# Kernel tuning notes

Measured on AMD Instinct MI355X. Metric: run time of the kernel, lower is better.

## Reference

```python
import jax, jax.numpy as jnp
import numpy as np

N_NODES = 1_000_000
HIDDEN = 256
NUM_GRAPHS = 1024
EPS = 1e-6


def setup_inputs() -> dict:
    key = jax.random.key(0)
    k1, k2 = jax.random.split(key)
    x = jax.random.normal(k1, (N_NODES, HIDDEN), dtype=jnp.float32)
    batch = jnp.sort(jax.random.randint(k2, (N_NODES,), 0, NUM_GRAPHS, dtype=jnp.int64))
    weight = jnp.ones((HIDDEN,), dtype=jnp.float32)
    return {"x": x, "batch": batch, "weight": weight}


def reference(x, batch, weight):
    # scatter_mean(x**2, batch, dim=0): per-graph mean of squared features
    seg_sum = jax.ops.segment_sum(x * x, batch, num_segments=NUM_GRAPHS)  # [G, H]
    counts = jax.ops.segment_sum(jnp.ones((x.shape[0],), x.dtype), batch,
                                 num_segments=NUM_GRAPHS)  # [G]
    seg_mean = seg_sum / jnp.maximum(counts, 1.0)[:, None]  # [G, H]
    rms_squared = seg_mean[batch]  # gather back to nodes: [N, H]
    rms = jnp.sqrt(jnp.mean(rms_squared, axis=-1, keepdims=True) + EPS)  # [N, 1]
    return weight * (x / rms)
```

## Files before the change

### kernel.cpp

```cpp
#include <hip/hip_runtime.h>

#define HIDDEN 256
#define NGRAPH 1024
#define EPS 1e-6f
#define STAGE_ROWS 152

typedef float f32x4 __attribute__((ext_vector_type(4)));

__global__ __launch_bounds__(512) void k_fused(
    const float* __restrict__ x, const int* __restrict__ batch,
    const float* __restrict__ w, float* __restrict__ out, int n_nodes) {

    __shared__ float smem[STAGE_ROWS * HIDDEN + 8];

    const int g    = (int)blockIdx.x;
    const int tid  = (int)threadIdx.x;
    const int lane = tid & 63;
    const int wid  = tid >> 6;

    int lo = 0, hi = n_nodes;
    while (lo < hi) { int m = (lo + hi) >> 1; if (batch[m] < g) lo = m + 1; else hi = m; }
    const int start = lo;
    int lo2 = start, hi2 = n_nodes;
    while (lo2 < hi2) { int m = (lo2 + hi2) >> 1; if (batch[m] < g + 1) lo2 = m + 1; else hi2 = m; }
    const int count = lo2 - start;
    if (count <= 0) return;

    const int nsweep = (count + 63) >> 6;

    float acc = 0.0f;
    for (int s = 0; s < nsweep; ++s) {
        const int base = (s << 6) + (wid << 3);
        if (base + 8 <= count) {
            f32x4 v[8];
            #pragma unroll
            for (int k = 0; k < 8; ++k)
                v[k] = *reinterpret_cast<const f32x4*>(
                    x + (size_t)(start + base + k) * HIDDEN + (size_t)lane * 4);
            if (base + 8 <= STAGE_ROWS) {
                #pragma unroll
                for (int k = 0; k < 8; ++k)
                    *reinterpret_cast<f32x4*>(
                        &smem[(base + k) * HIDDEN + lane * 4]) = v[k];
            }
            #pragma unroll
            for (int k = 0; k < 8; ++k)
                acc += v[k].x * v[k].x + v[k].y * v[k].y + v[k].z * v[k].z + v[k].w * v[k].w;
        } else {
            for (int r = base; r < count; ++r) {
                const f32x4 v = *reinterpret_cast<const f32x4*>(
                    x + (size_t)(start + r) * HIDDEN + (size_t)lane * 4);
                acc += v.x * v.x + v.y * v.y + v.z * v.z + v.w * v.w;
            }
        }
    }
    #pragma unroll
    for (int off = 32; off > 0; off >>= 1)
        acc += __shfl_xor(acc, off);
    if (lane == 0) smem[STAGE_ROWS * HIDDEN + wid] = acc;
    __syncthreads();

    float total = 0.0f;
    #pragma unroll
    for (int k = 0; k < 8; ++k) total += smem[STAGE_ROWS * HIDDEN + k];
    const float mean = total / ((float)count * (float)HIDDEN);
    const float rr   = 1.0f / sqrtf(mean + EPS);

    const f32x4 wv = *reinterpret_cast<const f32x4*>(w + (size_t)lane * 4);
    for (int s = nsweep - 1; s >= 0; --s) {
        const int base = (s << 6) + (wid << 3);
        if (base + 8 <= count) {
            f32x4 v[8];
            if (base + 8 <= STAGE_ROWS) {
                #pragma unroll
                for (int k = 0; k < 8; ++k)
                    v[k] = *reinterpret_cast<const f32x4*>(
                        &smem[(base + k) * HIDDEN + lane * 4]);
            } else {
                #pragma unroll
                for (int k = 0; k < 8; ++k)
                    v[k] = __builtin_nontemporal_load(reinterpret_cast<const f32x4*>(
                        x + (size_t)(start + base + k) * HIDDEN + (size_t)lane * 4));
            }
            #pragma unroll
            for (int k = 0; k < 8; ++k) {
                f32x4 o;
                o.x = v[k].x * wv.x * rr;
                o.y = v[k].y * wv.y * rr;
                o.z = v[k].z * wv.z * rr;
                o.w = v[k].w * wv.w * rr;
                __builtin_nontemporal_store(o, reinterpret_cast<f32x4*>(
                    out + (size_t)(start + base + k) * HIDDEN + (size_t)lane * 4));
            }
        } else {
            for (int r = base; r < count; ++r) {
                const f32x4 v = __builtin_nontemporal_load(reinterpret_cast<const f32x4*>(
                    x + (size_t)(start + r) * HIDDEN + (size_t)lane * 4));
                f32x4 o;
                o.x = v.x * wv.x * rr;
                o.y = v.y * wv.y * rr;
                o.z = v.z * wv.z * rr;
                o.w = v.w * wv.w * rr;
                __builtin_nontemporal_store(o, reinterpret_cast<f32x4*>(
                    out + (size_t)(start + r) * HIDDEN + (size_t)lane * 4));
            }
        }
    }
}

extern "C" void kernel_launch(void* const* d_in, const int* in_sizes, int n_in,
                              void* d_out, int out_size, void* d_ws, size_t ws_size,
                              hipStream_t stream) {
    const float* x     = (const float*)d_in[0];
    const int*   batch = (const int*)d_in[1];
    const float* w     = (const float*)d_in[2];
    float*       out   = (float*)d_out;
    const int n_nodes  = in_sizes[1];

    k_fused<<<NGRAPH, 512, 0, stream>>>(x, batch, w, out, n_nodes);
}
```

Before: 443.4 us.

## Stage segment rows in registers plus smaller LDS buffer to avoid re-reads

The kernel now caches the first two 64-row sweeps of each graph segment in LDS and the next five sweeps in per-thread registers (40 f32x4 per thread), rather than 152 rows in LDS. The normalize pass writes those staged rows straight from registers or LDS and only re-reads the rows beyond them from global memory. Launch bounds now request 2 blocks per CU. Segments average about 977 rows, so most rows are still read twice. The goal is to stage more of each segment (448 rows versus 152) and cut HBM re-reads, at the cost of high register pressure that may cause spills or limit occupancy.

```diff
diff --git a/kernel.cpp b/kernel.cpp
--- a/kernel.cpp
+++ b/kernel.cpp
@@ -3,15 +3,21 @@
 #define HIDDEN 256
 #define NGRAPH 1024
 #define EPS 1e-6f
-#define STAGE_ROWS 152
+#define LDS_SWEEPS 2
+#define REG_SWEEPS 5
+#define STAGE_SWEEPS (LDS_SWEEPS + REG_SWEEPS)
 
 typedef float f32x4 __attribute__((ext_vector_type(4)));
 
-__global__ __launch_bounds__(512) void k_fused(
+__device__ __forceinline__ float ssum(const f32x4 v) {
+    return v.x * v.x + v.y * v.y + v.z * v.z + v.w * v.w;
+}
+
+__global__ __launch_bounds__(512, 2) void k_fused(
     const float* __restrict__ x, const int* __restrict__ batch,
     const float* __restrict__ w, float* __restrict__ out, int n_nodes) {
 
-    __shared__ float smem[STAGE_ROWS * HIDDEN + 8];
+    __shared__ float smem[LDS_SWEEPS * 64 * HIDDEN + 8];
 
     const int g    = (int)blockIdx.x;
     const int tid  = (int)threadIdx.x;
@@ -29,7 +35,45 @@
     const int nsweep = (count + 63) >> 6;
 
     float acc = 0.0f;
-    for (int s = 0; s < nsweep; ++s) {
+    f32x4 rv[REG_SWEEPS][8];
+
+    #pragma unroll
+    for (int s = 0; s < LDS_SWEEPS; ++s) {
+        const int base = (s << 6) + (wid << 3);
+        if (base + 8 <= count) {
+            f32x4 v[8];
+            #pragma unroll
+            for (int k = 0; k < 8; ++k)
+                v[k] = __builtin_nontemporal_load(reinterpret_cast<const f32x4*>(
+                    x + (size_t)(start + base + k) * HIDDEN + (size_t)lane * 4));
+            #pragma unroll
+            for (int k = 0; k < 8; ++k)
+                *reinterpret_cast<f32x4*>(&smem[(base + k) * HIDDEN + lane * 4]) = v[k];
+            #pragma unroll
+            for (int k = 0; k < 8; ++k) acc += ssum(v[k]);
+        } else {
+            for (int r = base; r < count; ++r)
+                acc += ssum(*reinterpret_cast<const f32x4*>(
+                    x + (size_t)(start + r) * HIDDEN + (size_t)lane * 4));
+        }
+    }
+    #pragma unroll
+    for (int j = 0; j < REG_SWEEPS; ++j) {
+        const int base = ((LDS_SWEEPS + j) << 6) + (wid << 3);
+        if (base + 8 <= count) {
+            #pragma unroll
+            for (int k = 0; k < 8; ++k)
+                rv[j][k] = __builtin_nontemporal_load(reinterpret_cast<const f32x4*>(
+                    x + (size_t)(start + base + k) * HIDDEN + (size_t)lane * 4));
+            #pragma unroll
+            for (int k = 0; k < 8; ++k) acc += ssum(rv[j][k]);
+        } else {
+            for (int r = base; r < count; ++r)
+                acc += ssum(*reinterpret_cast<const f32x4*>(
+                    x + (size_t)(start + r) * HIDDEN + (size_t)lane * 4));
+        }
+    }
+    for (int s = STAGE_SWEEPS; s < nsweep; ++s) {
         const int base = (s << 6) + (wid << 3);
         if (base + 8 <= count) {
             f32x4 v[8];
@@ -37,58 +81,41 @@
             for (int k = 0; k < 8; ++k)
                 v[k] = *reinterpret_cast<const f32x4*>(
                     x + (size_t)(start + base + k) * HIDDEN + (size_t)lane * 4);
-            if (base + 8 <= STAGE_ROWS) {
-                #pragma unroll
-                for (int k = 0; k < 8; ++k)
-                    *reinterpret_cast<f32x4*>(
-                        &smem[(base + k) * HIDDEN + lane * 4]) = v[k];
-            }
             #pragma unroll
-            for (int k = 0; k < 8; ++k)
-                acc += v[k].x * v[k].x + v[k].y * v[k].y + v[k].z * v[k].z + v[k].w * v[k].w;
+            for (int k = 0; k < 8; ++k) acc += ssum(v[k]);
         } else {
-            for (int r = base; r < count; ++r) {
-                const f32x4 v = *reinterpret_cast<const f32x4*>(
-                    x + (size_t)(start + r) * HIDDEN + (size_t)lane * 4);
-                acc += v.x * v.x + v.y * v.y + v.z * v.z + v.w * v.w;
-            }
+            for (int r = base; r < count; ++r)
+                acc += ssum(*reinterpret_cast<const f32x4*>(
+                    x + (size_t)(start + r) * HIDDEN + (size_t)lane * 4));
         }
     }
+
     #pragma unroll
     for (int off = 32; off > 0; off >>= 1)
         acc += __shfl_xor(acc, off);
-    if (lane == 0) smem[STAGE_ROWS * HIDDEN + wid] = acc;
+    if (lane == 0) smem[LDS_SWEEPS * 64 * HIDDEN + wid] = acc;
     __syncthreads();
 
     float total = 0.0f;
     #pragma unroll
-    for (int k = 0; k < 8; ++k) total += smem[STAGE_ROWS * HIDDEN + k];
+    for (int k = 0; k < 8; ++k) total += smem[LDS_SWEEPS * 64 * HIDDEN + k];
     const float mean = total / ((float)count * (float)HIDDEN);
     const float rr   = 1.0f / sqrtf(mean + EPS);
 
     const f32x4 wv = *reinterpret_cast<const f32x4*>(w + (size_t)lane * 4);
-    for (int s = nsweep - 1; s >= 0; --s) {
+
+    for (int s = nsweep - 1; s >= STAGE_SWEEPS; --s) {
         const int base = (s << 6) + (wid << 3);
         if (base + 8 <= count) {
             f32x4 v[8];
-            if (base + 8 <= STAGE_ROWS) {
-                #pragma unroll
-                for (int k = 0; k < 8; ++k)
-                    v[k] = *reinterpret_cast<const f32x4*>(
-                        &smem[(base + k) * HIDDEN + lane * 4]);
-            } else {
-                #pragma unroll
-                for (int k = 0; k < 8; ++k)
-                    v[k] = __builtin_nontemporal_load(reinterpret_cast<const f32x4*>(
-                        x + (size_t)(start + base + k) * HIDDEN + (size_t)lane * 4));
-            }
+            #pragma unroll
+            for (int k = 0; k < 8; ++k)
+                v[k] = __builtin_nontemporal_load(reinterpret_cast<const f32x4*>(
+                    x + (size_t)(start + base + k) * HIDDEN + (size_t)lane * 4));
             #pragma unroll
             for (int k = 0; k < 8; ++k) {
-                f32x4 o;
-                o.x = v[k].x * wv.x * rr;
-                o.y = v[k].y * wv.y * rr;
-                o.z = v[k].z * wv.z * rr;
-                o.w = v[k].w * wv.w * rr;
+                f32x4 o = { v[k].x * wv.x * rr, v[k].y * wv.y * rr,
+                            v[k].z * wv.z * rr, v[k].w * wv.w * rr };
                 __builtin_nontemporal_store(o, reinterpret_cast<f32x4*>(
                     out + (size_t)(start + base + k) * HIDDEN + (size_t)lane * 4));
             }
@@ -96,11 +123,54 @@
             for (int r = base; r < count; ++r) {
                 const f32x4 v = __builtin_nontemporal_load(reinterpret_cast<const f32x4*>(
                     x + (size_t)(start + r) * HIDDEN + (size_t)lane * 4));
-                f32x4 o;
-                o.x = v.x * wv.x * rr;
-                o.y = v.y * wv.y * rr;
-                o.z = v.z * wv.z * rr;
-                o.w = v.w * wv.w * rr;
+                f32x4 o = { v.x * wv.x * rr, v.y * wv.y * rr,
+                            v.z * wv.z * rr, v.w * wv.w * rr };
+                __builtin_nontemporal_store(o, reinterpret_cast<f32x4*>(
+                    out + (size_t)(start + r) * HIDDEN + (size_t)lane * 4));
+            }
+        }
+    }
+    #pragma unroll
+    for (int j = REG_SWEEPS - 1; j >= 0; --j) {
+        const int base = ((LDS_SWEEPS + j) << 6) + (wid << 3);
+        if (base + 8 <= count) {
+            #pragma unroll
+            for (int k = 0; k < 8; ++k) {
+                f32x4 o = { rv[j][k].x * wv.x * rr, rv[j][k].y * wv.y * rr,
+                            rv[j][k].z * wv.z * rr, rv[j][k].w * wv.w * rr };
+                __builtin_nontemporal_store(o, reinterpret_cast<f32x4*>(
+                    out + (size_t)(start + base + k) * HIDDEN + (size_t)lane * 4));
+            }
+        } else {
+            for (int r = base; r < count; ++r) {
+                const f32x4 v = __builtin_nontemporal_load(reinterpret_cast<const f32x4*>(
+                    x + (size_t)(start + r) * HIDDEN + (size_t)lane * 4));
+                f32x4 o = { v.x * wv.x * rr, v.y * wv.y * rr,
+                            v.z * wv.z * rr, v.w * wv.w * rr };
+                __builtin_nontemporal_store(o, reinterpret_cast<f32x4*>(
+                    out + (size_t)(start + r) * HIDDEN + (size_t)lane * 4));
+            }
+        }
+    }
+    #pragma unroll
+    for (int s = LDS_SWEEPS - 1; s >= 0; --s) {
+        const int base = (s << 6) + (wid << 3);
+        if (base + 8 <= count) {
+            #pragma unroll
+            for (int k = 0; k < 8; ++k) {
+                const f32x4 v = *reinterpret_cast<const f32x4*>(
+                    &smem[(base + k) * HIDDEN + lane * 4]);
+                f32x4 o = { v.x * wv.x * rr, v.y * wv.y * rr,
+                            v.z * wv.z * rr, v.w * wv.w * rr };
+                __builtin_nontemporal_store(o, reinterpret_cast<f32x4*>(
+                    out + (size_t)(start + base + k) * HIDDEN + (size_t)lane * 4));
+            }
+        } else {
+            for (int r = base; r < count; ++r) {
+                const f32x4 v = __builtin_nontemporal_load(reinterpret_cast<const f32x4*>(
+                    x + (size_t)(start + r) * HIDDEN + (size_t)lane * 4));
+                f32x4 o = { v.x * wv.x * rr, v.y * wv.y * rr,
+                            v.z * wv.z * rr, v.w * wv.w * rr };
                 __builtin_nontemporal_store(o, reinterpret_cast<f32x4*>(
                     out + (size_t)(start + r) * HIDDEN + (size_t)lane * 4));
             }
```

Result: slower. 501.8 us (+13.2%).
